# Optimization experiments

Measured on AMD Instinct MI355X. Metric: run time of the kernel, lower is better.

Reference implementation:

```python
import jax, jax.numpy as jnp
import numpy as np

D = 1024
H = 16
HD = D // H


def quant_linear(x, W, b):
    # global abs-max fake quant, then linear (W is [out, in] like torch)
    scale = jnp.abs(x).max() / 127.0 + 1e-8
    xq = jnp.clip(jnp.round(x / scale), -128.0, 127.0) * scale
    return xq @ W.T + b


def rmsnorm(x, w, eps=1e-6):
    ms = jnp.mean(x * x, axis=-1, keepdims=True)
    return w * (x * jax.lax.rsqrt(ms + eps))


def setup_inputs() -> dict:
    key = jax.random.key(0)
    ks = jax.random.split(key, 20)
    def lin(k, out_f, in_f):
        bound = 1.0 / np.sqrt(in_f)
        kw, kb = jax.random.split(k)
        W = jax.random.uniform(kw, (out_f, in_f), jnp.float32, -bound, bound)
        b = jax.random.uniform(kb, (out_f,), jnp.float32, -bound, bound)
        return W, b
    x = jax.random.normal(ks[0], (4, 2048, D), jnp.float32)
    h_prev = jax.random.normal(ks[1], (4, 2048, D), jnp.float32)
    rec_W, rec_b = lin(ks[2], D, D)
    in_proj_w = jax.random.normal(ks[3], (3 * D, D), jnp.float32) * (1.0 / np.sqrt(D))
    in_proj_b = jnp.zeros((3 * D,), jnp.float32)
    out_w, out_b = lin(ks[4], D, D)
    w1_W, w1_b = lin(ks[5], 4 * D, D)
    w2_W, w2_b = lin(ks[6], 4 * D, D)
    w3_W, w3_b = lin(ks[7], D, 4 * D)
    # depthwise conv1d: torch weight [D, 1, 5]
    cb = 1.0 / np.sqrt(5)
    conv_w = jax.random.uniform(ks[8], (D, 1, 5), jnp.float32, -cb, cb)
    conv_b = jax.random.uniform(ks[9], (D,), jnp.float32, -cb, cb)
    return dict(x=x, h_prev=h_prev,
                norm1_w=jnp.ones((D,), jnp.float32), norm2_w=jnp.ones((D,), jnp.float32),
                decay=jnp.full((D,), -0.2, jnp.float32),
                rec_W=rec_W, rec_b=rec_b,
                in_proj_w=in_proj_w, in_proj_b=in_proj_b, out_w=out_w, out_b=out_b,
                conv_w=conv_w, conv_b=conv_b,
                w1_W=w1_W, w1_b=w1_b, w2_W=w2_W, w2_b=w2_b, w3_W=w3_W, w3_b=w3_b)


def reference(x, h_prev, norm1_w, norm2_w, decay, rec_W, rec_b,
              in_proj_w, in_proj_b, out_w, out_b, conv_w, conv_b,
              w1_W, w1_b, w2_W, w2_b, w3_W, w3_b):
    B, S, _ = x.shape
    nx = rmsnorm(x, norm1_w)
    # decay-gated recurrence (single step)
    h_rec = jnp.tanh(quant_linear(nx, rec_W, rec_b) + jnp.exp(decay) * h_prev)
    # multi-head self-attention (torch MultiheadAttention, batch_first)
    qkv = nx @ in_proj_w.T + in_proj_b  # [B,S,3D]
    q, k, v = jnp.split(qkv, 3, axis=-1)
    q = q.reshape(B, S, H, HD)
    k = k.reshape(B, S, H, HD)
    v = v.reshape(B, S, H, HD)
    scores = jnp.einsum('bqhd,bkhd->bhqk', q, k) / np.sqrt(HD)
    attn = jax.nn.softmax(scores, axis=-1)
    h_attn = jnp.einsum('bhqk,bkhd->bqhd', attn, v).reshape(B, S, D)
    h_attn = h_attn @ out_w.T + out_b
    # depthwise conv along sequence
    xc = jnp.swapaxes(nx, 1, 2)  # [B,D,S]
    hc = jax.lax.conv_general_dilated(xc, conv_w, window_strides=(1,), padding=[(2, 2)],
                                      feature_group_count=D,
                                      dimension_numbers=('NCH', 'OIH', 'NCH'))
    h_conv = jnp.swapaxes(hc + conv_b[None, :, None], 1, 2)
    x = x + h_rec + h_attn + h_conv
    # SwiGLU FFN with fake-quant linears
    nx2 = rmsnorm(x, norm2_w)
    ff = quant_linear(jax.nn.silu(quant_linear(nx2, w1_W, w1_b)) * quant_linear(nx2, w2_W, w2_b), w3_W, w3_b)
    x = x + ff
    return (x, h_rec)
```

## Files before the change

kernel.cpp:

```cpp
#include <hip/hip_runtime.h>
#include <stdint.h>

#define DD 1024
#define SS 2048
#define HH 16
#define HDD 64
#define NTOK 8192

typedef unsigned short u16;
typedef __attribute__((ext_vector_type(8))) short bf16x8;
typedef __attribute__((ext_vector_type(4))) float f32x4;
typedef __attribute__((ext_vector_type(4))) u16 u16x4;
typedef __attribute__((address_space(1))) unsigned int u32a1;
typedef __attribute__((address_space(3))) unsigned int u32a3;

__device__ __forceinline__ float bf2f(u16 u){
  union { float f; unsigned v; } c; c.v = ((unsigned)u) << 16; return c.f;
}
__device__ __forceinline__ u16 f2bf(float f){
  unsigned x = __float_as_uint(f);
  x = (x + 0x7fffu + ((x >> 16) & 1u)) >> 16;
  return (u16)x;
}
__device__ __forceinline__ void async16(const u16* g, u16* l){
  __builtin_amdgcn_global_load_lds((const u32a1*)g, (u32a3*)l, 16, 0, 0);
}
__device__ __forceinline__ int vswz(int row){
  return (((row & 7) ^ ((row >> 3) & 7)) << 4);
}
__device__ __forceinline__ unsigned cvtpk(float lo, float hi){
  unsigned r;
  asm("v_cvt_pk_bf16_f32 %0, %1, %2" : "=v"(r) : "v"(lo), "v"(hi));
  return r;
}


__global__ __launch_bounds__(256) void f32_to_bf16_kernel(
    const float* __restrict__ in, u16* __restrict__ out, int n)
{
  int i = (blockIdx.x * 256 + threadIdx.x) * 4;
  if (i >= n) return;
  float4 v = *(const float4*)(in + i);
  u16x4 o; o.x = f2bf(v.x); o.y = f2bf(v.y); o.z = f2bf(v.z); o.w = f2bf(v.w);
  *(u16x4*)(out + i) = o;
}

__global__ __launch_bounds__(256) void rmsnorm_absmax_kernel(
    const float* __restrict__ xin, const float* __restrict__ wgt,
    u16* __restrict__ nxo, float* __restrict__ pmax)
{
  const int row = blockIdx.x, t = threadIdx.x;
  const int w = t >> 6, l = t & 63;
  float4 xv = *(const float4*)(xin + (size_t)row * DD + t * 4);
  float ss = xv.x*xv.x + xv.y*xv.y + xv.z*xv.z + xv.w*xv.w;
  #pragma unroll
  for (int m = 1; m < 64; m <<= 1) ss += __shfl_xor(ss, m, 64);
  __shared__ float red[4];
  __shared__ float redm[4];
  if (l == 0) red[w] = ss;
  __syncthreads();
  float tot = red[0] + red[1] + red[2] + red[3];
  float rstd = rsqrtf(tot * (1.f / DD) + 1e-6f);
  float4 wv = *(const float4*)(wgt + t * 4);
  float o0 = xv.x * rstd * wv.x;
  float o1 = xv.y * rstd * wv.y;
  float o2 = xv.z * rstd * wv.z;
  float o3 = xv.w * rstd * wv.w;
  u16x4 ov; ov.x = f2bf(o0); ov.y = f2bf(o1); ov.z = f2bf(o2); ov.w = f2bf(o3);
  *(u16x4*)(nxo + (size_t)row * DD + t * 4) = ov;
  float lm = fmaxf(fmaxf(fabsf(o0), fabsf(o1)), fmaxf(fabsf(o2), fabsf(o3)));
  #pragma unroll
  for (int m = 1; m < 64; m <<= 1) lm = fmaxf(lm, __shfl_xor(lm, m, 64));
  if (l == 0) redm[w] = lm;
  __syncthreads();
  if (t == 0)
    pmax[row] = fmaxf(fmaxf(redm[0], redm[1]), fmaxf(redm[2], redm[3]));
}

__global__ __launch_bounds__(1024) void amax_reduce_kernel(
    const float* __restrict__ p, int n, unsigned* __restrict__ amax)
{
  const int t = threadIdx.x;
  float m = 0.f;
  for (int i = t; i < n; i += 1024) m = fmaxf(m, p[i]);
  #pragma unroll
  for (int msk = 1; msk < 64; msk <<= 1) m = fmaxf(m, __shfl_xor(m, msk, 64));
  __shared__ float red[16];
  if ((t & 63) == 0) red[t >> 6] = m;
  __syncthreads();
  if (t == 0){
    float mm = red[0];
    #pragma unroll
    for (int i = 1; i < 16; i++) mm = fmaxf(mm, red[i]);
    *amax = __float_as_uint(mm);
  }
}

__global__ __launch_bounds__(256) void quantize_kernel(
    const u16* __restrict__ in, u16* __restrict__ outq,
    const unsigned* __restrict__ amax, int n)
{
  int i = (blockIdx.x * 256 + threadIdx.x) * 8;
  if (i >= n) return;
  float am = __uint_as_float(*amax);
  float scale = am / 127.f + 1e-8f;
  float inv = 1.f / scale;
  uint4 a = *(const uint4*)(in + i);
  u16* u = (u16*)&a;
  #pragma unroll
  for (int j = 0; j < 8; j++){
    float v = bf2f(u[j]);
    float q = rintf(v * inv);
    q = fminf(127.f, fmaxf(-128.f, q));
    u[j] = f2bf(q * scale);
  }
  *(uint4*)(outq + i) = a;
}

template<int MODE>
__global__ __launch_bounds__(256) void gemm_bt(
    const u16* __restrict__ A, const u16* __restrict__ Wt,
    const float* __restrict__ bias, int M, int N, int K,
    void* __restrict__ out,
    const float* __restrict__ e0, const float* __restrict__ e1,
    const float* __restrict__ e2, const float* __restrict__ e3,
    const u16* __restrict__ eb0, float* __restrict__ pmax)
{
  __shared__ __align__(16) u16 Ash[128 * 32];
  __shared__ __align__(16) u16 Bsh[128 * 32];
  const int t = threadIdx.x, w = t >> 6, l = t & 63;
  const int brow = blockIdx.y * 128, bcol = blockIdx.x * 128;
  const int wr = w >> 1, wc = w & 1;
  f32x4 acc[4][4] = {};

  const u16* Ab = A + (size_t)brow * K;
  const u16* Bb = Wt + (size_t)bcol * K;
  const int r4 = t >> 2, c8 = (t & 3) * 8;

  for (int k0 = 0; k0 < K; k0 += 32){
    #pragma unroll
    for (int j = 0; j < 2; j++){
      async16(Ab + (size_t)(j * 64 + r4) * K + k0 + c8, &Ash[(j * 64 + r4) * 32 + c8]);
      async16(Bb + (size_t)(j * 64 + r4) * K + k0 + c8, &Bsh[(j * 64 + r4) * 32 + c8]);
    }
    __syncthreads();
    bf16x8 af[4], bfr[4];
    #pragma unroll
    for (int m = 0; m < 4; m++)
      af[m] = *(const bf16x8*)&Ash[(wr * 64 + m * 16 + (l & 15)) * 32 + (l >> 4) * 8];
    #pragma unroll
    for (int n = 0; n < 4; n++)
      bfr[n] = *(const bf16x8*)&Bsh[(wc * 64 + n * 16 + (l & 15)) * 32 + (l >> 4) * 8];
    #pragma unroll
    for (int m = 0; m < 4; m++)
      #pragma unroll
      for (int n = 0; n < 4; n++)
        acc[m][n] = __builtin_amdgcn_mfma_f32_16x16x32_bf16(af[m], bfr[n], acc[m][n], 0, 0, 0);
    __syncthreads();
  }

  float localmax = 0.f;
  #pragma unroll
  for (int m = 0; m < 4; m++){
    #pragma unroll
    for (int n = 0; n < 4; n++){
      #pragma unroll
      for (int r = 0; r < 4; r++){
        const int row = brow + wr * 64 + m * 16 + (l >> 4) * 4 + r;
        const int col = bcol + wc * 64 + n * 16 + (l & 15);
        const size_t idx = (size_t)row * N + col;
        float v = acc[m][n][r] + bias[col];
        if constexpr (MODE == 0){
          ((u16*)out)[idx] = f2bf(v);
        } else if constexpr (MODE == 1){
          v = tanhf(v + expf(e0[col]) * e1[idx]);
          ((float*)out)[idx] = v;
        } else if constexpr (MODE == 2){
          const int s = row & (SS - 1);
          float hc = e3[col];
          const u16* np = eb0 + idx;
          #pragma unroll
          for (int j = 0; j < 5; j++){
            int sn = s + j - 2;
            if (sn >= 0 && sn < SS) hc += bf2f(np[(j - 2) * DD]) * e2[col * 5 + j];
          }
          ((float*)out)[idx] = v + e0[idx] + e1[idx] + hc;
        } else if constexpr (MODE == 3){
          float h1v = bf2f(eb0[idx]);
          float g = h1v / (1.f + expf(-h1v)) * v;
          ((u16*)out)[idx] = f2bf(g);
          localmax = fmaxf(localmax, fabsf(g));
        } else {
          ((float*)out)[idx] += v;
        }
      }
    }
  }
  if constexpr (MODE == 3){
    #pragma unroll
    for (int msk = 1; msk < 64; msk <<= 1)
      localmax = fmaxf(localmax, __shfl_xor(localmax, msk, 64));
    __shared__ float wmax[4];
    if (l == 0) wmax[w] = localmax;
    __syncthreads();
    if (t == 0)
      pmax[blockIdx.y * gridDim.x + blockIdx.x] =
          fmaxf(fmaxf(wmax[0], wmax[1]), fmaxf(wmax[2], wmax[3]));
  }
}

__global__ __launch_bounds__(256) void attn_kernel(
    const u16* __restrict__ qkv, u16* __restrict__ attn_out)
{
  const int qb = blockIdx.x;
  const int bh = blockIdx.y;
  const int h = bh & (HH - 1), b = bh >> 4;
  const int t = threadIdx.x, w = t >> 6, l = t & 63;
  const int lm = l & 15, lh = l >> 4;
  const int tok0 = b * SS;
  const size_t rstr = 3 * DD;

  __shared__ __align__(16) u16 Ksh[64 * 64];
  __shared__ __align__(16) u16 Vsh[64 * 64];

  const int qr0 = qb * 128 + w * 32;
  bf16x8 qf[2][2];
  #pragma unroll
  for (int qt = 0; qt < 2; qt++){
    const u16* qp = qkv + (size_t)(tok0 + qr0 + qt * 16 + lm) * rstr + h * HDD + lh * 8;
    qf[qt][0] = *(const bf16x8*)qp;
    qf[qt][1] = *(const bf16x8*)(qp + 32);
  }
  f32x4 acc_o[2][4] = {};
  float mrun[2] = {-1e30f, -1e30f};
  float lrun[2] = {0.f, 0.f};

  for (int kv0 = 0; kv0 < SS; kv0 += 64){
    #pragma unroll
    for (int j = 0; j < 2; j++){
      const int krl = j * 32 + (t >> 3);
      const int c8 = (t & 7) * 8;
      const size_t rowb = (size_t)(tok0 + kv0 + krl) * rstr + h * HDD + c8;
      uint4 kv4 = *(const uint4*)(qkv + rowb + DD);
      *(uint4*)((char*)Ksh + (((krl * 64 + c8) * 2) ^ ((krl & 7) << 4))) = kv4;
      uint4 vv4 = *(const uint4*)(qkv + rowb + 2 * DD);
      const u16* vs = (const u16*)&vv4;
      #pragma unroll
      for (int i = 0; i < 8; i++){
        const int vr = c8 + i;
        *(u16*)((char*)Vsh + (((vr * 64 + krl) * 2) ^ vswz(vr))) = vs[i];
      }
    }
    __syncthreads();

    unsigned pk[2][4][2];
    #pragma unroll
    for (int qt = 0; qt < 2; qt++){
      f32x4 sc[4];
      #pragma unroll
      for (int n = 0; n < 4; n++){
        f32x4 z = {};
        #pragma unroll
        for (int kk = 0; kk < 2; kk++){
          const int krow = n * 16 + lm;
          bf16x8 kf = *(const bf16x8*)((const char*)Ksh +
              (((krow * 64 + kk * 32 + lh * 8) * 2) ^ ((krow & 7) << 4)));
          z = __builtin_amdgcn_mfma_f32_16x16x32_bf16(kf, qf[qt][kk], z, 0, 0, 0);
        }
        sc[n] = z;
      }
      float m0 = sc[0][0];
      #pragma unroll
      for (int n = 0; n < 4; n++)
        #pragma unroll
        for (int r = 0; r < 4; r++) m0 = fmaxf(m0, sc[n][r]);
      m0 = fmaxf(m0, __shfl_xor(m0, 16, 64));
      m0 = fmaxf(m0, __shfl_xor(m0, 32, 64));
      m0 *= 0.125f;
      float mn = fmaxf(mrun[qt], m0);
      float al = __expf(mrun[qt] - mn);
      mrun[qt] = mn;
      lrun[qt] *= al;
      #pragma unroll
      for (int r = 0; r < 4; r++){
        float alr = __shfl(al, lh * 4 + r, 64);
        #pragma unroll
        for (int n = 0; n < 4; n++) acc_o[qt][n][r] *= alr;
      }
      float rs = 0.f;
      #pragma unroll
      for (int n = 0; n < 4; n++)
        #pragma unroll
        for (int r = 0; r < 4; r++){
          float p = __expf(fmaf(sc[n][r], 0.125f, -mn));
          sc[n][r] = p;
          rs += p;
        }
      rs += __shfl_xor(rs, 16, 64);
      rs += __shfl_xor(rs, 32, 64);
      lrun[qt] += rs;
      #pragma unroll
      for (int n = 0; n < 4; n++){
        pk[qt][n][0] = cvtpk(sc[n][0], sc[n][1]);
        pk[qt][n][1] = cvtpk(sc[n][2], sc[n][3]);
      }
    }

    #pragma unroll
    for (int kk = 0; kk < 2; kk++){
      bf16x8 pA[2];
      #pragma unroll
      for (int qt = 0; qt < 2; qt++){
        union { bf16x8 v; unsigned u[4]; } pa;
        #pragma unroll
        for (int w4 = 0; w4 < 4; w4++){
          const int src = lm + 16 * (2 * (lh & 1) + (w4 >> 1));
          unsigned a0 = (unsigned)__shfl((int)pk[qt][2 * kk + 0][w4 & 1], src, 64);
          unsigned a1 = (unsigned)__shfl((int)pk[qt][2 * kk + 1][w4 & 1], src, 64);
          pa.u[w4] = (lh >> 1) ? a1 : a0;
        }
        pA[qt] = pa.v;
      }
      #pragma unroll
      for (int n = 0; n < 4; n++){
        const int vr = n * 16 + lm;
        bf16x8 vf = *(const bf16x8*)((const char*)Vsh +
            (((vr * 64 + kk * 32 + lh * 8) * 2) ^ vswz(vr)));
        acc_o[0][n] = __builtin_amdgcn_mfma_f32_16x16x32_bf16(pA[0], vf, acc_o[0][n], 0, 0, 0);
        acc_o[1][n] = __builtin_amdgcn_mfma_f32_16x16x32_bf16(pA[1], vf, acc_o[1][n], 0, 0, 0);
      }
    }
    __syncthreads();
  }

  #pragma unroll
  for (int qt = 0; qt < 2; qt++){
    const float inv = 1.f / lrun[qt];
    #pragma unroll
    for (int r = 0; r < 4; r++){
      const float invr = __shfl(inv, lh * 4 + r, 64);
      const int row = tok0 + qr0 + qt * 16 + lh * 4 + r;
      #pragma unroll
      for (int n = 0; n < 4; n++)
        attn_out[(size_t)row * DD + h * HDD + n * 16 + lm] = f2bf(acc_o[qt][n][r] * invr);
    }
  }
}


extern "C" void kernel_launch(void* const* d_in, const int* in_sizes, int n_in,
                              void* d_out, int out_size, void* d_ws, size_t ws_size,
                              hipStream_t stream)
{
  (void)in_sizes; (void)n_in; (void)out_size; (void)ws_size;
  const float* x       = (const float*)d_in[0];
  const float* h_prev  = (const float*)d_in[1];
  const float* norm1_w = (const float*)d_in[2];
  const float* norm2_w = (const float*)d_in[3];
  const float* decay   = (const float*)d_in[4];
  const float* rec_W   = (const float*)d_in[5];
  const float* rec_b   = (const float*)d_in[6];
  const float* inp_W   = (const float*)d_in[7];
  const float* inp_b   = (const float*)d_in[8];
  const float* out_W   = (const float*)d_in[9];
  const float* out_b   = (const float*)d_in[10];
  const float* conv_w  = (const float*)d_in[11];
  const float* conv_b  = (const float*)d_in[12];
  const float* w1_W    = (const float*)d_in[13];
  const float* w1_b    = (const float*)d_in[14];
  const float* w2_W    = (const float*)d_in[15];
  const float* w2_b    = (const float*)d_in[16];
  const float* w3_W    = (const float*)d_in[17];
  const float* w3_b    = (const float*)d_in[18];

  const size_t NDe = (size_t)NTOK * DD;
  float* out_x = (float*)d_out;
  float* out_h = (float*)d_out + NDe;

  char* ws = (char*)d_ws;
  unsigned* amax1 = (unsigned*)ws;
  unsigned* amax2 = amax1 + 1;
  unsigned* amax3 = amax1 + 2;
  size_t off = 256;
  u16* Wrec = (u16*)(ws + off); off += (size_t)DD * DD * 2;
  u16* Winp = (u16*)(ws + off); off += (size_t)3 * DD * DD * 2;
  u16* Wout = (u16*)(ws + off); off += (size_t)DD * DD * 2;
  u16* W1   = (u16*)(ws + off); off += (size_t)4 * DD * DD * 2;
  u16* W2   = (u16*)(ws + off); off += (size_t)4 * DD * DD * 2;
  u16* W3   = (u16*)(ws + off); off += (size_t)4 * DD * DD * 2;
  u16* nx   = (u16*)(ws + off); off += NDe * 2;
  u16* xq   = (u16*)(ws + off); off += NDe * 2;
  u16* big  = (u16*)(ws + off); off += (size_t)NTOK * 4096 * 2;
  float* pmax1 = (float*)(ws + off); off += NTOK * 4;
  float* pmax2 = (float*)(ws + off); off += NTOK * 4;
  float* pmax3 = (float*)(ws + off); off += 2048 * 4;
  u16* qkvp    = big;
  u16* attnout = big + (size_t)NTOK * 3 * DD;

  f32_to_bf16_kernel<<<dim3(1024),  dim3(256), 0, stream>>>(rec_W, Wrec, DD * DD);
  f32_to_bf16_kernel<<<dim3(3072),  dim3(256), 0, stream>>>(inp_W, Winp, 3 * DD * DD);
  f32_to_bf16_kernel<<<dim3(1024),  dim3(256), 0, stream>>>(out_W, Wout, DD * DD);
  f32_to_bf16_kernel<<<dim3(4096),  dim3(256), 0, stream>>>(w1_W, W1, 4 * DD * DD);
  f32_to_bf16_kernel<<<dim3(4096),  dim3(256), 0, stream>>>(w2_W, W2, 4 * DD * DD);
  f32_to_bf16_kernel<<<dim3(4096),  dim3(256), 0, stream>>>(w3_W, W3, 4 * DD * DD);

  rmsnorm_absmax_kernel<<<dim3(NTOK), dim3(256), 0, stream>>>(x, norm1_w, nx, pmax1);
  amax_reduce_kernel<<<dim3(1), dim3(1024), 0, stream>>>(pmax1, NTOK, amax1);
  quantize_kernel<<<dim3(4096), dim3(256), 0, stream>>>(nx, xq, amax1, (int)NDe);

  gemm_bt<1><<<dim3(8, 64), dim3(256), 0, stream>>>(xq, Wrec, rec_b, NTOK, DD, DD,
      out_h, decay, h_prev, nullptr, nullptr, nullptr, nullptr);
  gemm_bt<0><<<dim3(24, 64), dim3(256), 0, stream>>>(nx, Winp, inp_b, NTOK, 3 * DD, DD,
      qkvp, nullptr, nullptr, nullptr, nullptr, nullptr, nullptr);
  attn_kernel<<<dim3(16, 64), dim3(256), 0, stream>>>(qkvp, attnout);
  gemm_bt<2><<<dim3(8, 64), dim3(256), 0, stream>>>(attnout, Wout, out_b, NTOK, DD, DD,
      out_x, x, out_h, conv_w, conv_b, nx, nullptr);

  rmsnorm_absmax_kernel<<<dim3(NTOK), dim3(256), 0, stream>>>(out_x, norm2_w, nx, pmax2);
  amax_reduce_kernel<<<dim3(1), dim3(1024), 0, stream>>>(pmax2, NTOK, amax2);
  quantize_kernel<<<dim3(4096), dim3(256), 0, stream>>>(nx, xq, amax2, (int)NDe);
  gemm_bt<0><<<dim3(32, 64), dim3(256), 0, stream>>>(xq, W1, w1_b, NTOK, 4 * DD, DD,
      big, nullptr, nullptr, nullptr, nullptr, nullptr, nullptr);
  gemm_bt<3><<<dim3(32, 64), dim3(256), 0, stream>>>(xq, W2, w2_b, NTOK, 4 * DD, DD,
      big, nullptr, nullptr, nullptr, nullptr, big, pmax3);
  amax_reduce_kernel<<<dim3(1), dim3(1024), 0, stream>>>(pmax3, 2048, amax3);
  quantize_kernel<<<dim3(16384), dim3(256), 0, stream>>>(big, big, amax3, NTOK * 4096);
  gemm_bt<4><<<dim3(8, 64), dim3(256), 0, stream>>>(big, W3, w3_b, NTOK, DD, 4 * DD,
      out_x, nullptr, nullptr, nullptr, nullptr, nullptr, nullptr);
}
```

Measured before the change: 1.078 ms.

## Fuse W1 and W2 GEMMs into one dual-accumulator SwiGLU kernel; swizzle attention grid

Replaces the two separate FFN up-projection GEMMs (one writing h1 in bf16, the second reading it back for the SiLU gate) with a single kernel that loads each A tile once and accumulates both W1 and W2 products, applying SiLU-gating and the abs-max reduction in the epilogue. This removes a full 8192x4096 bf16 write and read of the intermediate and halves A-tile traffic. The cost is double the accumulator registers (launch bounds of 2 blocks per unit) and more shared memory per block, which may reduce occupancy. The attention kernel's block index is also remapped so that consecutive workgroups spread across heads and batches.

```diff
diff --git a/kernel.cpp b/kernel.cpp
--- a/kernel.cpp
+++ b/kernel.cpp
@@ -159,7 +159,6 @@
     __syncthreads();
   }
 
-  float localmax = 0.f;
   #pragma unroll
   for (int m = 0; m < 4; m++){
     #pragma unroll
@@ -185,35 +184,99 @@
             if (sn >= 0 && sn < SS) hc += bf2f(np[(j - 2) * DD]) * e2[col * 5 + j];
           }
           ((float*)out)[idx] = v + e0[idx] + e1[idx] + hc;
-        } else if constexpr (MODE == 3){
-          float h1v = bf2f(eb0[idx]);
-          float g = h1v / (1.f + expf(-h1v)) * v;
-          ((u16*)out)[idx] = f2bf(g);
-          localmax = fmaxf(localmax, fabsf(g));
         } else {
           ((float*)out)[idx] += v;
         }
       }
     }
   }
-  if constexpr (MODE == 3){
-    #pragma unroll
-    for (int msk = 1; msk < 64; msk <<= 1)
-      localmax = fmaxf(localmax, __shfl_xor(localmax, msk, 64));
-    __shared__ float wmax[4];
-    if (l == 0) wmax[w] = localmax;
-    __syncthreads();
-    if (t == 0)
-      pmax[blockIdx.y * gridDim.x + blockIdx.x] =
-          fmaxf(fmaxf(wmax[0], wmax[1]), fmaxf(wmax[2], wmax[3]));
-  }
+  (void)pmax;
+}
+
+__global__ __launch_bounds__(256, 2) void gemm_dual_swiglu(
+    const u16* __restrict__ A, const u16* __restrict__ W1t,
+    const u16* __restrict__ W2t,
+    const float* __restrict__ b1, const float* __restrict__ b2,
+    int M, int N, int K,
+    u16* __restrict__ out, float* __restrict__ pmax)
+{
+  __shared__ __align__(16) u16 Ash[128 * 32];
+  __shared__ __align__(16) u16 B1sh[128 * 32];
+  __shared__ __align__(16) u16 B2sh[128 * 32];
+  const int t = threadIdx.x, w = t >> 6, l = t & 63;
+  const int brow = blockIdx.y * 128, bcol = blockIdx.x * 128;
+  const int wr = w >> 1, wc = w & 1;
+  f32x4 acc1[4][4] = {};
+  f32x4 acc2[4][4] = {};
+
+  const u16* Ab  = A   + (size_t)brow * K;
+  const u16* B1b = W1t + (size_t)bcol * K;
+  const u16* B2b = W2t + (size_t)bcol * K;
+  const int r4 = t >> 2, c8 = (t & 3) * 8;
+
+  for (int k0 = 0; k0 < K; k0 += 32){
+    #pragma unroll
+    for (int j = 0; j < 2; j++){
+      async16(Ab  + (size_t)(j * 64 + r4) * K + k0 + c8, &Ash [(j * 64 + r4) * 32 + c8]);
+      async16(B1b + (size_t)(j * 64 + r4) * K + k0 + c8, &B1sh[(j * 64 + r4) * 32 + c8]);
+      async16(B2b + (size_t)(j * 64 + r4) * K + k0 + c8, &B2sh[(j * 64 + r4) * 32 + c8]);
+    }
+    __syncthreads();
+    bf16x8 af[4];
+    #pragma unroll
+    for (int m = 0; m < 4; m++)
+      af[m] = *(const bf16x8*)&Ash[(wr * 64 + m * 16 + (l & 15)) * 32 + (l >> 4) * 8];
+    #pragma unroll
+    for (int n = 0; n < 4; n++){
+      const int bo = (wc * 64 + n * 16 + (l & 15)) * 32 + (l >> 4) * 8;
+      bf16x8 bf1 = *(const bf16x8*)&B1sh[bo];
+      #pragma unroll
+      for (int m = 0; m < 4; m++)
+        acc1[m][n] = __builtin_amdgcn_mfma_f32_16x16x32_bf16(af[m], bf1, acc1[m][n], 0, 0, 0);
+      bf16x8 bf2 = *(const bf16x8*)&B2sh[bo];
+      #pragma unroll
+      for (int m = 0; m < 4; m++)
+        acc2[m][n] = __builtin_amdgcn_mfma_f32_16x16x32_bf16(af[m], bf2, acc2[m][n], 0, 0, 0);
+    }
+    __syncthreads();
+  }
+
+  float localmax = 0.f;
+  #pragma unroll
+  for (int m = 0; m < 4; m++){
+    #pragma unroll
+    for (int n = 0; n < 4; n++){
+      #pragma unroll
+      for (int r = 0; r < 4; r++){
+        const int row = brow + wr * 64 + m * 16 + (l >> 4) * 4 + r;
+        const int col = bcol + wc * 64 + n * 16 + (l & 15);
+        const size_t idx = (size_t)row * N + col;
+        float v1 = acc1[m][n][r] + b1[col];
+        float v2 = acc2[m][n][r] + b2[col];
+        float g = v1 / (1.f + expf(-v1)) * v2;
+        out[idx] = f2bf(g);
+        localmax = fmaxf(localmax, fabsf(g));
+      }
+    }
+  }
+  #pragma unroll
+  for (int msk = 1; msk < 64; msk <<= 1)
+    localmax = fmaxf(localmax, __shfl_xor(localmax, msk, 64));
+  __shared__ float wmax[4];
+  if (l == 0) wmax[w] = localmax;
+  __syncthreads();
+  if (t == 0)
+    pmax[blockIdx.y * gridDim.x + blockIdx.x] =
+        fmaxf(fmaxf(wmax[0], wmax[1]), fmaxf(wmax[2], wmax[3]));
 }
 
 __global__ __launch_bounds__(256) void attn_kernel(
     const u16* __restrict__ qkv, u16* __restrict__ attn_out)
 {
-  const int qb = blockIdx.x;
-  const int bh = blockIdx.y;
+  const int wg = blockIdx.y * gridDim.x + blockIdx.x;
+  const int swz = (wg & 7) * 128 + (wg >> 3);
+  const int qb = swz & 15;
+  const int bh = swz >> 4;
   const int h = bh & (HH - 1), b = bh >> 4;
   const int t = threadIdx.x, w = t >> 6, l = t & 63;
   const int lm = l & 15, lh = l >> 4;
@@ -419,10 +482,8 @@
   rmsnorm_absmax_kernel<<<dim3(NTOK), dim3(256), 0, stream>>>(out_x, norm2_w, nx, pmax2);
   amax_reduce_kernel<<<dim3(1), dim3(1024), 0, stream>>>(pmax2, NTOK, amax2);
   quantize_kernel<<<dim3(4096), dim3(256), 0, stream>>>(nx, xq, amax2, (int)NDe);
-  gemm_bt<0><<<dim3(32, 64), dim3(256), 0, stream>>>(xq, W1, w1_b, NTOK, 4 * DD, DD,
-      big, nullptr, nullptr, nullptr, nullptr, nullptr, nullptr);
-  gemm_bt<3><<<dim3(32, 64), dim3(256), 0, stream>>>(xq, W2, w2_b, NTOK, 4 * DD, DD,
-      big, nullptr, nullptr, nullptr, nullptr, big, pmax3);
+  gemm_dual_swiglu<<<dim3(32, 64), dim3(256), 0, stream>>>(xq, W1, W2, w1_b, w2_b,
+      NTOK, 4 * DD, DD, big, pmax3);
   amax_reduce_kernel<<<dim3(1), dim3(1024), 0, stream>>>(pmax3, 2048, amax3);
   quantize_kernel<<<dim3(16384), dim3(256), 0, stream>>>(big, big, amax3, NTOK * 4096);
   gemm_bt<4><<<dim3(8, 64), dim3(256), 0, stream>>>(big, W3, w3_b, NTOK, DD, 4 * DD,
```

New measurement: 1.009 ms. 1.07x faster.
